# Kernel tuning notes

Hardware: AMD Instinct MI355X
Metric: run time of the kernel (lower is better)

The kernel has to match this reference:

```python
import jax, jax.numpy as jnp
import numpy as np

B, N, F, A, E, D, V, L = 128, 36, 2048, 1024, 1024, 1024, 10000, 20


def setup_inputs() -> dict:
    key = jax.random.key(0)
    ks = jax.random.split(key, 24)
    s = 0.02
    image_features = jax.random.normal(ks[0], (B, N, F), jnp.float32)
    encoded_captions = jax.random.randint(ks[1], (B, L), 0, V, jnp.int32)
    caption_lengths = jax.random.randint(ks[2], (B, 1), 5, L + 1, jnp.int32)
    caption_lengths = caption_lengths.at[0, 0].set(L)  # ensure max decode len = L-1
    p = lambda k, shape: jax.random.normal(k, shape, jnp.float32) * s
    return {
        "image_features": image_features,
        "encoded_captions": encoded_captions,
        "caption_lengths": caption_lengths,
        "emb": jax.random.uniform(ks[3], (V, E), jnp.float32, -0.1, 0.1),
        "W1_ih": p(ks[4], (4 * D, E + F + D)),
        "W1_hh": p(ks[5], (4 * D, D)),
        "b1_ih": jnp.zeros((4 * D,), jnp.float32),
        "b1_hh": jnp.zeros((4 * D,), jnp.float32),
        "W2_ih": p(ks[6], (4 * D, F + D)),
        "W2_hh": p(ks[7], (4 * D, D)),
        "b2_ih": jnp.zeros((4 * D,), jnp.float32),
        "b2_hh": jnp.zeros((4 * D,), jnp.float32),
        "Wf": p(ks[8], (A, F)),
        "bf": jnp.zeros((A,), jnp.float32),
        "Wd": p(ks[9], (A, D)),
        "bd": jnp.zeros((A,), jnp.float32),
        "Wa": p(ks[10], (1, A)),
        "ba": jnp.zeros((1,), jnp.float32),
        "Wfc": jax.random.uniform(ks[11], (V, D), jnp.float32, -0.1, 0.1),
        "bfc": jnp.zeros((V,), jnp.float32),
    }


def _lstm_cell(x, h, c, Wih, Whh, bih, bhh):
    g = x @ Wih.T + bih + h @ Whh.T + bhh
    i, f, gg, o = jnp.split(g, 4, axis=-1)
    c2 = jax.nn.sigmoid(f) * c + jax.nn.sigmoid(i) * jnp.tanh(gg)
    h2 = jax.nn.sigmoid(o) * jnp.tanh(c2)
    return h2, c2


def reference(image_features, encoded_captions, caption_lengths, emb,
              W1_ih, W1_hh, b1_ih, b1_hh, W2_ih, W2_hh, b2_ih, b2_hh,
              Wf, bf, Wd, bd, Wa, ba, Wfc, bfc):
    lengths = caption_lengths[:, 0]
    sort_ind = jnp.argsort(-lengths)  # descending, as in torch sort
    feats = image_features[sort_ind]            # [B,N,F]
    caps = encoded_captions[sort_ind]           # [B,L]
    dec_len = lengths[sort_ind] - 1             # [B]
    feats_mean = feats.mean(axis=1)             # [B,F]
    embs = emb[caps]                            # [B,L,E]
    att1 = feats @ Wf.T + bf                    # [B,N,A] (constant per step)
    T = caps.shape[1] - 1
    d = feats.dtype
    h1 = jnp.zeros((caps.shape[0], W1_hh.shape[1]), d)
    c1, h2, c2 = h1, h1, h1

    def step(carry, xs):
        h1, c1, h2, c2 = carry
        emb_t, t = xs
        active = (t < dec_len)[:, None].astype(d)  # ragged batch mask
        x1 = jnp.concatenate([h2, feats_mean, emb_t], axis=1)
        nh1, nc1 = _lstm_cell(x1, h1, c1, W1_ih, W1_hh, b1_ih, b1_hh)
        h1 = active * nh1 + (1.0 - active) * h1
        c1 = active * nc1 + (1.0 - active) * c1
        # additive attention (dropout is identity at eval)
        att2 = h1 @ Wd.T + bd                   # [B,A]
        e = (jax.nn.relu(att1 + att2[:, None, :]) @ Wa.T + ba)[..., 0]  # [B,N]
        alpha = jax.nn.softmax(e, axis=1)
        awe = jnp.einsum('bnf,bn->bf', feats, alpha)
        x2 = jnp.concatenate([awe, h1], axis=1)
        nh2, nc2 = _lstm_cell(x2, h2, c2, W2_ih, W2_hh, b2_ih, b2_hh)
        h2 = active * nh2 + (1.0 - active) * h2
        c2 = active * nc2 + (1.0 - active) * c2
        preds = (h2 @ Wfc.T + bfc) * active     # zeros past decode_length
        return (h1, c1, h2, c2), preds

    xs = (jnp.swapaxes(embs[:, :T, :], 0, 1), jnp.arange(T))
    _, preds = jax.lax.scan(step, (h1, c1, h2, c2), xs)
    return jnp.transpose(preds, (1, 0, 2))      # [B,T,V]
```

## Files before the change

### kernel.cpp

```cpp
#include <hip/hip_runtime.h>
#include <hip/hip_bf16.h>
#include <math.h>

#define B   128
#define NN  36
#define FF  2048
#define AA  1024
#define EE  1024
#define DD  1024
#define VV  10000
#define LL  20
#define TT  19

typedef __attribute__((ext_vector_type(8))) short short8;
typedef __attribute__((ext_vector_type(4))) float floatx4;

__global__ __launch_bounds__(B) void sort_kernel(const int* __restrict__ cap_len,
                                                 int* __restrict__ sort_ind,
                                                 int* __restrict__ dec_len) {
    __shared__ int lsh[B];
    int i = threadIdx.x;
    lsh[i] = cap_len[i];
    __syncthreads();
    int li = lsh[i];
    int rank = 0;
    for (int j = 0; j < B; ++j) {
        int lj = lsh[j];
        rank += (lj > li) || (lj == li && j < i);
    }
    sort_ind[rank] = i;
    dec_len[rank]  = li - 1;
}

__global__ void pack_all_kernel(const float* __restrict__ W1_ih, const float* __restrict__ W1_hh,
                                const float* __restrict__ W2_ih, const float* __restrict__ W2_hh,
                                const float* __restrict__ Wd,    const float* __restrict__ Wfc,
                                const float* __restrict__ Wf,    const float* __restrict__ img,
                                const int* __restrict__ sort_ind,
                                __hip_bfloat16* __restrict__ W1dyn, __hip_bfloat16* __restrict__ W1fm,
                                __hip_bfloat16* __restrict__ W1emb, __hip_bfloat16* __restrict__ W2cat,
                                __hip_bfloat16* __restrict__ Wd_bf, __hip_bfloat16* __restrict__ Wfc_bf,
                                __hip_bfloat16* __restrict__ Wf_bf, __hip_bfloat16* __restrict__ feats_bf) {
    size_t idx = (size_t)blockIdx.x * 256 + threadIdx.x;
    if (idx < 8388608UL) {
        size_t i = idx; int n = i >> 11, k = i & 2047;
        float v = (k < 1024) ? W1_ih[(size_t)n * 4096 + k] : W1_hh[(size_t)n * 1024 + (k - 1024)];
        W1dyn[i] = __float2bfloat16(v);
    } else if (idx < 16777216UL) {
        size_t i = idx - 8388608UL; int n = i >> 11, k = i & 2047;
        W1fm[i] = __float2bfloat16(W1_ih[(size_t)n * 4096 + 1024 + k]);
    } else if (idx < 20971520UL) {
        size_t i = idx - 16777216UL; int n = i >> 10, k = i & 1023;
        W1emb[i] = __float2bfloat16(W1_ih[(size_t)n * 4096 + 3072 + k]);
    } else if (idx < 37748736UL) {
        size_t i = idx - 20971520UL; int n = i >> 12, k = i & 4095;
        float v = (k < 3072) ? W2_ih[(size_t)n * 3072 + k] : W2_hh[(size_t)n * 1024 + (k - 3072)];
        W2cat[i] = __float2bfloat16(v);
    } else if (idx < 38797312UL) {
        size_t i = idx - 37748736UL;
        Wd_bf[i] = __float2bfloat16(Wd[i]);
    } else if (idx < 49037312UL) {
        size_t i = idx - 38797312UL;
        Wfc_bf[i] = __float2bfloat16(Wfc[i]);
    } else if (idx < 51134464UL) {
        size_t i = idx - 49037312UL;
        Wf_bf[i] = __float2bfloat16(Wf[i]);
    } else {
        size_t i = idx - 51134464UL;
        int b = (int)(i / (NN * FF));
        int r = (int)(i % (NN * FF));
        feats_bf[i] = __float2bfloat16(img[(size_t)sort_ind[b] * (NN * FF) + r]);
    }
}

__global__ void fm_kernel(const float* __restrict__ img,
                          const int* __restrict__ sort_ind,
                          __hip_bfloat16* __restrict__ fmbf) {
    int i = blockIdx.x * 256 + threadIdx.x;
    int b = i >> 11;
    int f = i & 2047;
    const float* src = img + (size_t)sort_ind[b] * (NN * FF) + f;
    float s = 0.f;
#pragma unroll
    for (int n = 0; n < NN; ++n) s += src[n * FF];
    fmbf[i] = __float2bfloat16(s * (1.0f / NN));
}

__global__ void embcat_kernel(const float* __restrict__ emb,
                              const int* __restrict__ caps,
                              const int* __restrict__ sort_ind,
                              __hip_bfloat16* __restrict__ embcat) {
    int i = blockIdx.x * 256 + threadIdx.x;
    int row = i >> 10;
    int e = i & 1023;
    int t = row >> 7;
    int b = row & 127;
    int cap = caps[sort_ind[b] * LL + t];
    embcat[i] = __float2bfloat16(emb[(size_t)cap * EE + e]);
}

#define BM 128
#define BN 64
#define BK 64
#define LDS_K 72

template<int EPI>
__device__ __forceinline__ void gemm_core(
        short (*As)[LDS_K], short (*Wsm)[LDS_K],
        int bm, int bn, int k0,
        const __hip_bfloat16* __restrict__ A, int lda,
        const __hip_bfloat16* __restrict__ W, int ldw,
        float* __restrict__ C, int ldc,
        int N, int Kc,
        const float* __restrict__ bias,
        const int* __restrict__ dec_len) {
    const int tid  = threadIdx.x;
    const int lane = tid & 63;
    const int wv   = tid >> 6;
    const int quad = lane >> 4;
    const int l15  = lane & 15;
    const int wm   = (wv >> 1) * 64;
    const int wn   = (wv & 1) * 32;
    const int srow = tid >> 3;
    const int scol = (tid & 7) * 8;

    floatx4 acc[4][2];
#pragma unroll
    for (int i = 0; i < 4; ++i)
#pragma unroll
        for (int j = 0; j < 2; ++j)
            acc[i][j] = (floatx4){0.f, 0.f, 0.f, 0.f};

    const __hip_bfloat16* Aptr = A + (size_t)(bm + srow) * lda + k0 + scol;
    const __hip_bfloat16* Wptr = W + k0 + scol;

    for (int kt = 0; kt < Kc; kt += BK) {
#pragma unroll
        for (int p = 0; p < 4; ++p) {
            floatx4 v = *(const floatx4*)(Aptr + (size_t)(p * 32) * lda + kt);
            *(floatx4*)(&As[p * 32 + srow][scol]) = v;
        }
#pragma unroll
        for (int p = 0; p < 2; ++p) {
            int gw = bn + p * 32 + srow;
            floatx4 v;
            if (EPI != 3 || gw < N)
                v = *(const floatx4*)(Wptr + (size_t)gw * ldw + kt);
            else
                v = (floatx4){0.f, 0.f, 0.f, 0.f};
            *(floatx4*)(&Wsm[p * 32 + srow][scol]) = v;
        }
        __syncthreads();
#pragma unroll
        for (int ks = 0; ks < 2; ++ks) {
            short8 af[4], bw[2];
#pragma unroll
            for (int i = 0; i < 4; ++i)
                af[i] = *(const short8*)(&As[wm + i * 16 + l15][ks * 32 + quad * 8]);
#pragma unroll
            for (int j = 0; j < 2; ++j)
                bw[j] = *(const short8*)(&Wsm[wn + j * 16 + l15][ks * 32 + quad * 8]);
#pragma unroll
            for (int i = 0; i < 4; ++i)
#pragma unroll
                for (int j = 0; j < 2; ++j)
                    acc[i][j] = __builtin_amdgcn_mfma_f32_16x16x32_bf16(
                        af[i], bw[j], acc[i][j], 0, 0, 0);
        }
        __syncthreads();
    }

#pragma unroll
    for (int i = 0; i < 4; ++i) {
        int m = bm + wm + i * 16 + quad * 4;
#pragma unroll
        for (int j = 0; j < 2; ++j) {
            int n = bn + wn + j * 16 + l15;
            if (EPI == 3 && n >= N) continue;
#pragma unroll
            for (int r = 0; r < 4; ++r) {
                float v = acc[i][j][r];
                if (EPI == 3) {
                    int row = m + r;
                    int tt = row >> 7;
                    int bb = row & 127;
                    bool act = tt < dec_len[bb];
                    C[(size_t)bb * (TT * VV) + (size_t)tt * VV + n] =
                        act ? (v + bias[n]) : 0.f;
                } else if (EPI == 2) {
                    ((__hip_bfloat16*)C)[(size_t)(m + r) * ldc + n] = __float2bfloat16(v);
                } else {
                    C[(size_t)(m + r) * ldc + n] = v;
                }
            }
        }
    }
}

template<int EPI>
__global__ __launch_bounds__(256) void gemm_bf16(
        const __hip_bfloat16* __restrict__ A, int lda,
        const __hip_bfloat16* __restrict__ W, int ldw,
        float* __restrict__ C, int ldc, size_t pstride,
        int N, int Kc,
        const float* __restrict__ bias,
        const int* __restrict__ dec_len) {
    if (blockIdx.x * BN >= N) return;
    __shared__ __align__(16) short As[BM][LDS_K];
    __shared__ __align__(16) short Wsm[BN][LDS_K];
    gemm_core<EPI>(As, Wsm, blockIdx.y * BM, blockIdx.x * BN, blockIdx.z * Kc,
                   A, lda, W, ldw, C + (size_t)blockIdx.z * pstride, ldc,
                   N, Kc, bias, dec_len);
}

__global__ __launch_bounds__(256) void gemm_d3(
        const __hip_bfloat16* __restrict__ x2full,
        const __hip_bfloat16* __restrict__ Wd_bf,
        const __hip_bfloat16* __restrict__ W2cat,
        float* __restrict__ att2_part, size_t astride,
        float* __restrict__ g_part, size_t gstride) {
    __shared__ __align__(16) short As[BM][LDS_K];
    __shared__ __align__(16) short Wsm[BN][LDS_K];
    int idx = blockIdx.x;
    if (idx < 128) {
        int bx = idx & 15, z = idx >> 4;
        gemm_core<0>(As, Wsm, 0, bx * BN, z * 128,
                     x2full + 2048, 4096, Wd_bf, DD,
                     att2_part + (size_t)z * astride, AA,
                     AA, 128, nullptr, nullptr);
    } else {
        int j = idx - 128;
        int bx = j & 63, z = j >> 6;
        gemm_core<0>(As, Wsm, 0, bx * BN, 2048 + z * 512,
                     x2full, 4096, W2cat, 4096,
                     g_part + (size_t)(4 + z) * gstride, 4096,
                     4096, 512, nullptr, nullptr);
    }
}

template<int NZ>
__global__ void lstm_kernel(const float* __restrict__ gpart, size_t pstride,
                            const float* __restrict__ bih, const float* __restrict__ bhh,
                            const float* __restrict__ pre0, const float* __restrict__ pre1,
                            float* __restrict__ c,
                            __hip_bfloat16* __restrict__ hs1, int st1,
                            __hip_bfloat16* __restrict__ hs2, int st2,
                            __hip_bfloat16* __restrict__ hs3,
                            const int* __restrict__ dec_len, int t) {
    int idx = blockIdx.x * 256 + threadIdx.x;
    int b = idx >> 10;
    int d = idx & 1023;
    if (t >= dec_len[b]) return;
    float g[4];
#pragma unroll
    for (int gate = 0; gate < 4; ++gate) {
        size_t o = (size_t)b * 4096 + gate * 1024 + d;
        float s = bih[gate * 1024 + d] + bhh[gate * 1024 + d];
        if (pre0) s += pre0[o];
        if (pre1) s += pre1[o];
#pragma unroll
        for (int z = 0; z < NZ; ++z) s += gpart[z * pstride + o];
        g[gate] = s;
    }
    float si = 1.f / (1.f + expf(-g[0]));
    float sf = 1.f / (1.f + expf(-g[1]));
    float so = 1.f / (1.f + expf(-g[3]));
    float cc = sf * c[idx] + si * tanhf(g[2]);
    float hh = so * tanhf(cc);
    c[idx] = cc;
    __hip_bfloat16 hb = __float2bfloat16(hh);
    hs1[(size_t)b * st1 + d] = hb;
    hs2[(size_t)b * st2 + d] = hb;
    if (hs3) hs3[(size_t)b * 1024 + d] = hb;
}

__global__ __launch_bounds__(1024) void att_fused(
        const float* __restrict__ p, size_t pstride,
        const float* __restrict__ bf_,
        const float* __restrict__ bd_,
        float* __restrict__ av_g,
        const __hip_bfloat16* __restrict__ att1,
        const float* __restrict__ Wa,
        const __hip_bfloat16* __restrict__ feats,
        __hip_bfloat16* __restrict__ x2full) {
    int b = blockIdx.x;
    int tid = threadIdx.x;
    __shared__ float esh[NN];
    __shared__ float alpha[NN];

    {
        size_t o = (size_t)b * AA + tid;
        float s = bf_[tid] + bd_[tid];
#pragma unroll
        for (int z = 0; z < 8; ++z) s += p[z * pstride + o];
        av_g[o] = s;
    }
    __syncthreads();

    int wv = tid >> 6, lane = tid & 63;
    const float* avp = av_g + (size_t)b * AA + lane * 16;
    const float* wap = Wa + lane * 16;
    for (int n = wv; n < NN; n += 16) {
        const __hip_bfloat16* a1 = att1 + ((size_t)b * NN + n) * AA + lane * 16;
        float pacc = 0.f;
#pragma unroll
        for (int h = 0; h < 2; ++h) {
            short8 a8 = *(const short8*)(a1 + h * 8);
            floatx4 v0 = *(const floatx4*)(avp + h * 8);
            floatx4 v1 = *(const floatx4*)(avp + h * 8 + 4);
            floatx4 w0 = *(const floatx4*)(wap + h * 8);
            floatx4 w1 = *(const floatx4*)(wap + h * 8 + 4);
            float af[8];
#pragma unroll
            for (int q = 0; q < 8; ++q) {
                union { short s; __hip_bfloat16 b; } u; u.s = a8[q];
                af[q] = __bfloat162float(u.b);
            }
#pragma unroll
            for (int q = 0; q < 4; ++q) {
                pacc += fmaxf(af[q] + v0[q], 0.f) * w0[q];
                pacc += fmaxf(af[4 + q] + v1[q], 0.f) * w1[q];
            }
        }
        for (int off = 32; off; off >>= 1) pacc += __shfl_down(pacc, off);
        if (lane == 0) esh[n] = pacc;
    }
    __syncthreads();

    if (tid < 64) {
        float ev = (tid < NN) ? esh[tid] : -INFINITY;
        float m = ev;
        for (int off = 32; off; off >>= 1) m = fmaxf(m, __shfl_down(m, off));
        m = __shfl(m, 0);
        float ex = (tid < NN) ? expf(ev - m) : 0.f;
        float s = ex;
        for (int off = 32; off; off >>= 1) s += __shfl_down(s, off);
        s = __shfl(s, 0);
        if (tid < NN) alpha[tid] = ex / s;
    }
    __syncthreads();

    int f0 = tid * 2;
    const __hip_bfloat16* src = feats + (size_t)b * (NN * FF) + f0;
    float s0 = 0.f, s1 = 0.f;
#pragma unroll
    for (int n = 0; n < NN; ++n) {
        __hip_bfloat162 v = *(const __hip_bfloat162*)(src + n * FF);
        float al = alpha[n];
        s0 += al * __bfloat162float(v.x);
        s1 += al * __bfloat162float(v.y);
    }
    __hip_bfloat162 o;
    o.x = __float2bfloat16(s0);
    o.y = __float2bfloat16(s1);
    *(__hip_bfloat162*)(x2full + (size_t)b * 4096 + f0) = o;
}

extern "C" void kernel_launch(void* const* d_in, const int* in_sizes, int n_in,
                              void* d_out, int out_size, void* d_ws, size_t ws_size,
                              hipStream_t stream) {
    const float* img     = (const float*)d_in[0];
    const int*   caps    = (const int*)d_in[1];
    const int*   cap_len = (const int*)d_in[2];
    const float* emb     = (const float*)d_in[3];
    const float* W1_ih   = (const float*)d_in[4];
    const float* W1_hh   = (const float*)d_in[5];
    const float* b1_ih   = (const float*)d_in[6];
    const float* b1_hh   = (const float*)d_in[7];
    const float* W2_ih   = (const float*)d_in[8];
    const float* W2_hh   = (const float*)d_in[9];
    const float* b2_ih   = (const float*)d_in[10];
    const float* b2_hh   = (const float*)d_in[11];
    const float* Wf      = (const float*)d_in[12];
    const float* bf      = (const float*)d_in[13];
    const float* Wd      = (const float*)d_in[14];
    const float* bd      = (const float*)d_in[15];
    const float* Wa      = (const float*)d_in[16];
    const float* Wfc     = (const float*)d_in[18];
    const float* bfc     = (const float*)d_in[19];
    float* out = (float*)d_out;
    (void)in_sizes; (void)n_in; (void)out_size; (void)ws_size;

    char* ws = (char*)d_ws;
    size_t off = 0;
    auto alloc = [&](size_t bytes) -> void* {
        void* p = ws + off;
        off += (bytes + 255) & ~(size_t)255;
        return p;
    };
    int* sort_ind = (int*)alloc(B * sizeof(int));
    int* dec_len  = (int*)alloc(B * sizeof(int));
    __hip_bfloat16* W1dyn    = (__hip_bfloat16*)alloc((size_t)4096 * 2048 * 2);
    __hip_bfloat16* W1fm     = (__hip_bfloat16*)alloc((size_t)4096 * 2048 * 2);
    __hip_bfloat16* W1emb    = (__hip_bfloat16*)alloc((size_t)4096 * 1024 * 2);
    __hip_bfloat16* W2cat    = (__hip_bfloat16*)alloc((size_t)4096 * 4096 * 2);
    __hip_bfloat16* Wd_bf    = (__hip_bfloat16*)alloc((size_t)AA * DD * 2);
    __hip_bfloat16* Wfc_bf   = (__hip_bfloat16*)alloc((size_t)VV * DD * 2);
    __hip_bfloat16* Wf_bf    = (__hip_bfloat16*)alloc((size_t)AA * FF * 2);
    __hip_bfloat16* feats_bf = (__hip_bfloat16*)alloc((size_t)B * NN * FF * 2);
    __hip_bfloat16* att1_bf  = (__hip_bfloat16*)alloc((size_t)B * NN * AA * 2);
    __hip_bfloat16* fmbf     = (__hip_bfloat16*)alloc((size_t)B * 2048 * 2);
    __hip_bfloat16* embcat   = (__hip_bfloat16*)alloc((size_t)TT * B * EE * 2);
    __hip_bfloat16* h2hist   = (__hip_bfloat16*)alloc((size_t)TT * B * DD * 2);
    float* gpre_fm   = (float*)alloc((size_t)B * 4096 * 4);
    float* gpre_emb  = (float*)alloc((size_t)TT * B * 4096 * 4);
    float* g_part    = (float*)alloc((size_t)8 * B * 4096 * 4);
    float* att2_part = (float*)alloc((size_t)8 * B * AA * 4);
    float* av        = (float*)alloc((size_t)B * AA * 4);
    __hip_bfloat16* x1dyn  = (__hip_bfloat16*)alloc((size_t)B * 2048 * 2);
    __hip_bfloat16* x2full = (__hip_bfloat16*)alloc((size_t)B * 4096 * 2);
    float* c1 = (float*)alloc((size_t)B * DD * 4);
    float* c2 = (float*)alloc((size_t)B * DD * 4);

    const size_t gstride = (size_t)B * 4096;
    const size_t astride = (size_t)B * AA;

    sort_kernel<<<1, B, 0, stream>>>(cap_len, sort_ind, dec_len);
    pack_all_kernel<<<236608, 256, 0, stream>>>(
        W1_ih, W1_hh, W2_ih, W2_hh, Wd, Wfc, Wf, img, sort_ind,
        W1dyn, W1fm, W1emb, W2cat, Wd_bf, Wfc_bf, Wf_bf, feats_bf);
    fm_kernel<<<(B * 2048) / 256, 256, 0, stream>>>(img, sort_ind, fmbf);
    embcat_kernel<<<(TT * B * EE) / 256, 256, 0, stream>>>(emb, caps, sort_ind, embcat);
    hipMemsetAsync(x1dyn, 0, (size_t)B * 2048 * 2, stream);
    hipMemsetAsync(x2full, 0, (size_t)B * 4096 * 2, stream);
    hipMemsetAsync(c1, 0, (size_t)B * DD * 4, stream);
    hipMemsetAsync(c2, 0, (size_t)B * DD * 4, stream);
    hipMemsetAsync(h2hist, 0, (size_t)TT * B * DD * 2, stream);

    gemm_bf16<2><<<dim3(AA / BN, (B * NN) / BM, 1), 256, 0, stream>>>(
        feats_bf, FF, Wf_bf, FF, (float*)att1_bf, AA, 0, AA, FF, nullptr, nullptr);
    gemm_bf16<0><<<dim3(4096 / BN, 1, 1), 256, 0, stream>>>(
        fmbf, 2048, W1fm, 2048, gpre_fm, 4096, 0, 4096, 2048, nullptr, nullptr);
    gemm_bf16<0><<<dim3(4096 / BN, TT, 1), 256, 0, stream>>>(
        embcat, EE, W1emb, EE, gpre_emb, 4096, 0, 4096, EE, nullptr, nullptr);

    for (int t = 0; t < TT; ++t) {
        gemm_bf16<0><<<dim3(4096 / BN, 1, 4), 256, 0, stream>>>(
            x1dyn, 2048, W1dyn, 2048, g_part, 4096, gstride, 4096, 512,
            nullptr, nullptr);

        lstm_kernel<4><<<(B * DD) / 256, 256, 0, stream>>>(
            g_part, gstride, b1_ih, b1_hh,
            gpre_fm, gpre_emb + (size_t)t * B * 4096, c1,
            x1dyn + 1024, 2048, x2full + 2048, 4096, nullptr, dec_len, t);

        gemm_d3<<<128 + 256, 256, 0, stream>>>(
            x2full, Wd_bf, W2cat, att2_part, astride, g_part, gstride);

        att_fused<<<B, 1024, 0, stream>>>(att2_part, astride, bf, bd, av,
                                          att1_bf, Wa, feats_bf, x2full);

        gemm_bf16<0><<<dim3(4096 / BN, 1, 4), 256, 0, stream>>>(
            x2full, 4096, W2cat, 4096, g_part, 4096, gstride, 4096, 512,
            nullptr, nullptr);

        lstm_kernel<8><<<(B * DD) / 256, 256, 0, stream>>>(
            g_part, gstride, b2_ih, b2_hh, nullptr, nullptr, c2,
            x1dyn + 0, 2048, x2full + 3072, 4096,
            h2hist + (size_t)t * B * DD, dec_len, t);
    }

    gemm_bf16<3><<<dim3(160, TT, 1), 256, 0, stream>>>(
        h2hist, DD, Wfc_bf, DD, out, TT * VV, 0, VV, DD, bfc, dec_len);
}
```

Baseline: 1.602 ms.

## Vectorize setup conversion kernels, merge setup GEMMs, coalesce memsets

The weight and feature packing, the feature-mean and embedding-gather kernels now handle 8 or 4 elements per thread, using vector float loads and packed bf16 stores instead of scalar ones. The three one-off precompute GEMMs are merged into a single launch that picks its sub-problem from the block index. The separate memsets are folded into one by placing the zero-initialised buffers next to each other. The aim is to cut launch overhead and raise memory throughput in the setup phase, which moves a lot of fp32 weight data. It assumes every converted region is a multiple of 8 elements and 16-byte aligned, which holds for these shapes.

```diff
diff --git a/kernel.cpp b/kernel.cpp
--- a/kernel.cpp
+++ b/kernel.cpp
@@ -14,6 +14,18 @@
 
 typedef __attribute__((ext_vector_type(8))) short short8;
 typedef __attribute__((ext_vector_type(4))) float floatx4;
+
+__device__ __forceinline__ short f2bs(float x) {
+    union { __hip_bfloat16 b; short s; } u; u.b = __float2bfloat16(x); return u.s;
+}
+__device__ __forceinline__ void cvt8(const float* __restrict__ s, __hip_bfloat16* __restrict__ d) {
+    floatx4 a = *(const floatx4*)s;
+    floatx4 b = *(const floatx4*)(s + 4);
+    short8 o;
+    o[0] = f2bs(a[0]); o[1] = f2bs(a[1]); o[2] = f2bs(a[2]); o[3] = f2bs(a[3]);
+    o[4] = f2bs(b[0]); o[5] = f2bs(b[1]); o[6] = f2bs(b[2]); o[7] = f2bs(b[3]);
+    *(short8*)d = o;
+}
 
 __global__ __launch_bounds__(B) void sort_kernel(const int* __restrict__ cap_len,
                                                  int* __restrict__ sort_ind,
@@ -41,62 +53,74 @@
                                 __hip_bfloat16* __restrict__ W1emb, __hip_bfloat16* __restrict__ W2cat,
                                 __hip_bfloat16* __restrict__ Wd_bf, __hip_bfloat16* __restrict__ Wfc_bf,
                                 __hip_bfloat16* __restrict__ Wf_bf, __hip_bfloat16* __restrict__ feats_bf) {
-    size_t idx = (size_t)blockIdx.x * 256 + threadIdx.x;
+    size_t idx = ((size_t)blockIdx.x * 256 + threadIdx.x) * 8;
+    const float* src;
+    __hip_bfloat16* dst;
     if (idx < 8388608UL) {
-        size_t i = idx; int n = i >> 11, k = i & 2047;
-        float v = (k < 1024) ? W1_ih[(size_t)n * 4096 + k] : W1_hh[(size_t)n * 1024 + (k - 1024)];
-        W1dyn[i] = __float2bfloat16(v);
+        size_t i = idx; int n = (int)(i >> 11), k = (int)(i & 2047);
+        src = (k < 1024) ? (W1_ih + (size_t)n * 4096 + k) : (W1_hh + (size_t)n * 1024 + (k - 1024));
+        dst = W1dyn + i;
     } else if (idx < 16777216UL) {
-        size_t i = idx - 8388608UL; int n = i >> 11, k = i & 2047;
-        W1fm[i] = __float2bfloat16(W1_ih[(size_t)n * 4096 + 1024 + k]);
+        size_t i = idx - 8388608UL; int n = (int)(i >> 11), k = (int)(i & 2047);
+        src = W1_ih + (size_t)n * 4096 + 1024 + k;
+        dst = W1fm + i;
     } else if (idx < 20971520UL) {
-        size_t i = idx - 16777216UL; int n = i >> 10, k = i & 1023;
-        W1emb[i] = __float2bfloat16(W1_ih[(size_t)n * 4096 + 3072 + k]);
+        size_t i = idx - 16777216UL; int n = (int)(i >> 10), k = (int)(i & 1023);
+        src = W1_ih + (size_t)n * 4096 + 3072 + k;
+        dst = W1emb + i;
     } else if (idx < 37748736UL) {
-        size_t i = idx - 20971520UL; int n = i >> 12, k = i & 4095;
-        float v = (k < 3072) ? W2_ih[(size_t)n * 3072 + k] : W2_hh[(size_t)n * 1024 + (k - 3072)];
-        W2cat[i] = __float2bfloat16(v);
+        size_t i = idx - 20971520UL; int n = (int)(i >> 12), k = (int)(i & 4095);
+        src = (k < 3072) ? (W2_ih + (size_t)n * 3072 + k) : (W2_hh + (size_t)n * 1024 + (k - 3072));
+        dst = W2cat + i;
     } else if (idx < 38797312UL) {
         size_t i = idx - 37748736UL;
-        Wd_bf[i] = __float2bfloat16(Wd[i]);
+        src = Wd + i;  dst = Wd_bf + i;
     } else if (idx < 49037312UL) {
         size_t i = idx - 38797312UL;
-        Wfc_bf[i] = __float2bfloat16(Wfc[i]);
+        src = Wfc + i; dst = Wfc_bf + i;
     } else if (idx < 51134464UL) {
         size_t i = idx - 49037312UL;
-        Wf_bf[i] = __float2bfloat16(Wf[i]);
+        src = Wf + i;  dst = Wf_bf + i;
     } else {
         size_t i = idx - 51134464UL;
         int b = (int)(i / (NN * FF));
         int r = (int)(i % (NN * FF));
-        feats_bf[i] = __float2bfloat16(img[(size_t)sort_ind[b] * (NN * FF) + r]);
-    }
+        src = img + (size_t)sort_ind[b] * (NN * FF) + r;
+        dst = feats_bf + i;
+    }
+    cvt8(src, dst);
 }
 
 __global__ void fm_kernel(const float* __restrict__ img,
                           const int* __restrict__ sort_ind,
                           __hip_bfloat16* __restrict__ fmbf) {
-    int i = blockIdx.x * 256 + threadIdx.x;
+    int i = (blockIdx.x * 256 + threadIdx.x) * 4;
     int b = i >> 11;
     int f = i & 2047;
     const float* src = img + (size_t)sort_ind[b] * (NN * FF) + f;
-    float s = 0.f;
-#pragma unroll
-    for (int n = 0; n < NN; ++n) s += src[n * FF];
-    fmbf[i] = __float2bfloat16(s * (1.0f / NN));
+    floatx4 s = (floatx4){0.f, 0.f, 0.f, 0.f};
+#pragma unroll
+    for (int n = 0; n < NN; ++n) {
+        floatx4 v = *(const floatx4*)(src + (size_t)n * FF);
+        s[0] += v[0]; s[1] += v[1]; s[2] += v[2]; s[3] += v[3];
+    }
+    short o4[4];
+#pragma unroll
+    for (int q = 0; q < 4; ++q) o4[q] = f2bs(s[q] * (1.0f / NN));
+    *(uint2*)(fmbf + i) = *(uint2*)o4;
 }
 
 __global__ void embcat_kernel(const float* __restrict__ emb,
                               const int* __restrict__ caps,
                               const int* __restrict__ sort_ind,
                               __hip_bfloat16* __restrict__ embcat) {
-    int i = blockIdx.x * 256 + threadIdx.x;
-    int row = i >> 10;
-    int e = i & 1023;
+    size_t i = ((size_t)blockIdx.x * 256 + threadIdx.x) * 8;
+    int row = (int)(i >> 10);
+    int e = (int)(i & 1023);
     int t = row >> 7;
     int b = row & 127;
     int cap = caps[sort_ind[b] * LL + t];
-    embcat[i] = __float2bfloat16(emb[(size_t)cap * EE + e]);
+    cvt8(emb + (size_t)cap * EE + e, embcat + i);
 }
 
 #define BM 128
@@ -211,6 +235,33 @@
     gemm_core<EPI>(As, Wsm, blockIdx.y * BM, blockIdx.x * BN, blockIdx.z * Kc,
                    A, lda, W, ldw, C + (size_t)blockIdx.z * pstride, ldc,
                    N, Kc, bias, dec_len);
+}
+
+__global__ __launch_bounds__(256) void gemm_setup(
+        const __hip_bfloat16* __restrict__ feats_bf, const __hip_bfloat16* __restrict__ Wf_bf,
+        __hip_bfloat16* __restrict__ att1_bf,
+        const __hip_bfloat16* __restrict__ embcat,   const __hip_bfloat16* __restrict__ W1emb,
+        float* __restrict__ gpre_emb,
+        const __hip_bfloat16* __restrict__ fmbf,     const __hip_bfloat16* __restrict__ W1fm,
+        float* __restrict__ gpre_fm) {
+    __shared__ __align__(16) short As[BM][LDS_K];
+    __shared__ __align__(16) short Wsm[BN][LDS_K];
+    int idx = blockIdx.x;
+    if (idx < 576) {
+        gemm_core<2>(As, Wsm, (idx >> 4) * BM, (idx & 15) * BN, 0,
+                     feats_bf, FF, Wf_bf, FF, (float*)att1_bf, AA,
+                     AA, FF, nullptr, nullptr);
+    } else if (idx < 1792) {
+        int j = idx - 576;
+        gemm_core<0>(As, Wsm, (j >> 6) * BM, (j & 63) * BN, 0,
+                     embcat, EE, W1emb, EE, gpre_emb, 4096,
+                     4096, EE, nullptr, nullptr);
+    } else {
+        int j = idx - 1792;
+        gemm_core<0>(As, Wsm, 0, j * BN, 0,
+                     fmbf, 2048, W1fm, 2048, gpre_fm, 4096,
+                     4096, 2048, nullptr, nullptr);
+    }
 }
 
 __global__ __launch_bounds__(256) void gemm_d3(
@@ -401,38 +452,32 @@
     __hip_bfloat16* att1_bf  = (__hip_bfloat16*)alloc((size_t)B * NN * AA * 2);
     __hip_bfloat16* fmbf     = (__hip_bfloat16*)alloc((size_t)B * 2048 * 2);
     __hip_bfloat16* embcat   = (__hip_bfloat16*)alloc((size_t)TT * B * EE * 2);
-    __hip_bfloat16* h2hist   = (__hip_bfloat16*)alloc((size_t)TT * B * DD * 2);
     float* gpre_fm   = (float*)alloc((size_t)B * 4096 * 4);
     float* gpre_emb  = (float*)alloc((size_t)TT * B * 4096 * 4);
     float* g_part    = (float*)alloc((size_t)8 * B * 4096 * 4);
     float* att2_part = (float*)alloc((size_t)8 * B * AA * 4);
     float* av        = (float*)alloc((size_t)B * AA * 4);
+    char* zbase = (char*)alloc(0);
+    __hip_bfloat16* h2hist = (__hip_bfloat16*)alloc((size_t)TT * B * DD * 2);
     __hip_bfloat16* x1dyn  = (__hip_bfloat16*)alloc((size_t)B * 2048 * 2);
     __hip_bfloat16* x2full = (__hip_bfloat16*)alloc((size_t)B * 4096 * 2);
     float* c1 = (float*)alloc((size_t)B * DD * 4);
     float* c2 = (float*)alloc((size_t)B * DD * 4);
+    size_t zlen = (char*)alloc(0) - zbase;
 
     const size_t gstride = (size_t)B * 4096;
     const size_t astride = (size_t)B * AA;
 
     sort_kernel<<<1, B, 0, stream>>>(cap_len, sort_ind, dec_len);
-    pack_all_kernel<<<236608, 256, 0, stream>>>(
+    pack_all_kernel<<<29576, 256, 0, stream>>>(
         W1_ih, W1_hh, W2_ih, W2_hh, Wd, Wfc, Wf, img, sort_ind,
         W1dyn, W1fm, W1emb, W2cat, Wd_bf, Wfc_bf, Wf_bf, feats_bf);
-    fm_kernel<<<(B * 2048) / 256, 256, 0, stream>>>(img, sort_ind, fmbf);
-    embcat_kernel<<<(TT * B * EE) / 256, 256, 0, stream>>>(emb, caps, sort_ind, embcat);
-    hipMemsetAsync(x1dyn, 0, (size_t)B * 2048 * 2, stream);
-    hipMemsetAsync(x2full, 0, (size_t)B * 4096 * 2, stream);
-    hipMemsetAsync(c1, 0, (size_t)B * DD * 4, stream);
-    hipMemsetAsync(c2, 0, (size_t)B * DD * 4, stream);
-    hipMemsetAsync(h2hist, 0, (size_t)TT * B * DD * 2, stream);
-
-    gemm_bf16<2><<<dim3(AA / BN, (B * NN) / BM, 1), 256, 0, stream>>>(
-        feats_bf, FF, Wf_bf, FF, (float*)att1_bf, AA, 0, AA, FF, nullptr, nullptr);
-    gemm_bf16<0><<<dim3(4096 / BN, 1, 1), 256, 0, stream>>>(
-        fmbf, 2048, W1fm, 2048, gpre_fm, 4096, 0, 4096, 2048, nullptr, nullptr);
-    gemm_bf16<0><<<dim3(4096 / BN, TT, 1), 256, 0, stream>>>(
-        embcat, EE, W1emb, EE, gpre_emb, 4096, 0, 4096, EE, nullptr, nullptr);
+    fm_kernel<<<(B * 2048) / 4 / 256, 256, 0, stream>>>(img, sort_ind, fmbf);
+    embcat_kernel<<<(TT * B * EE) / 8 / 256, 256, 0, stream>>>(emb, caps, sort_ind, embcat);
+    hipMemsetAsync(zbase, 0, zlen, stream);
+
+    gemm_setup<<<1856, 256, 0, stream>>>(
+        feats_bf, Wf_bf, att1_bf, embcat, W1emb, gpre_emb, fmbf, W1fm, gpre_fm);
 
     for (int t = 0; t < TT; ++t) {
         gemm_bf16<0><<<dim3(4096 / BN, 1, 4), 256, 0, stream>>>(
```

Result: faster. 1.503 ms (-6.2%).
